# Kernel optimization log

Measured on AMD Instinct MI355X. Metric: run time of the kernel, lower is better.

## Reference

```python
import jax, jax.numpy as jnp
import numpy as np

B, D, T = 8, 256, 8192
N_Q, BINS = 8, 1024
COMMIT_W = 0.25

def setup_inputs() -> dict:
    key = jax.random.key(0)
    k1, k2 = jax.random.split(key)
    x = jax.random.normal(k1, (B, D, T), dtype=jnp.float32)
    codebooks = jax.random.normal(k2, (N_Q, BINS, D), dtype=jnp.float32)
    return {"x": x, "sample_rate": 16000, "codebooks": codebooks}

def _rvq(x_btd, codebooks):
    # x_btd: [B, T, D]; codebooks: [n_q, bins, D]
    def step(residual, cb):
        # nearest codebook entry under squared euclidean distance
        dots = jnp.einsum('btd,kd->btk', residual, cb)          # [B, T, K]
        cb_sq = jnp.sum(cb * cb, axis=-1)                        # [K]
        dist = cb_sq[None, None, :] - 2.0 * dots                 # argmin-equivalent distance
        idx = jnp.argmin(dist, axis=-1)                          # [B, T] int32
        q = cb[idx]                                              # [B, T, D] gather
        # commitment loss (codebook side detached, EnCodec style)
        loss = COMMIT_W * jnp.mean((jax.lax.stop_gradient(q) - residual) ** 2)
        # straight-through estimator
        q_ste = residual + jax.lax.stop_gradient(q - residual)
        return residual - q_ste, (q_ste, idx, loss)

    _, (qs, codes, losses) = jax.lax.scan(step, x_btd, codebooks)
    quantized = jnp.sum(qs, axis=0)                              # [B, T, D]
    return quantized, codes, losses

def reference(x, sample_rate, codebooks):
    n_q = codebooks.shape[0]
    bins = codebooks.shape[1]
    x_btd = jnp.transpose(x, (0, 2, 1))                          # [B, T, D]
    quantized_btd, codes, losses = _rvq(x_btd, codebooks)
    quantized = jnp.transpose(quantized_btd, (0, 2, 1))          # [B, D, T]
    bw_per_q = np.log2(bins) * sample_rate / 1000.0
    bw = jnp.asarray(n_q * bw_per_q, dtype=x.dtype)
    commit_loss = jnp.mean(losses)
    return quantized, codes, bw, commit_loss
```

## Files before the change

### kernel.cpp

```cpp
#include <hip/hip_runtime.h>
#include <math.h>

typedef _Float16 f16;
typedef f16 f16x8 __attribute__((ext_vector_type(8)));
typedef float f32x4 __attribute__((ext_vector_type(4)));

#define B_ 8
#define D_ 256
#define T_ 8192
#define NQ 8
#define KB 1024
#define TT 64
#define NTHR 512

#define OUT_CODES (B_ * D_ * T_)
#define OUT_BW (OUT_CODES + NQ * B_ * T_)
#define OUT_LOSS (OUT_BW + 1)

#define R_BYTES 65536
#define RED_OFF R_BYTES
#define REDI_OFF (RED_OFF + 1024)
#define WSUM_OFF (REDI_OFF + 1024)
#define LDS_TOTAL (WSUM_OFF + 32)

#define WS_HI (8192 * 4)
#define CBW_HALVES (NQ * 8 * KB * 32)
#define WS_LO (WS_HI + CBW_HALVES * 2)

__global__ void init_cbsq_kernel(const float* __restrict__ cb, const int* __restrict__ sr,
                                 float* __restrict__ csq, float* __restrict__ out) {
    int gid = blockIdx.x * blockDim.x + threadIdx.x;
    int row = gid >> 6;
    int lane = gid & 63;
    float4 v = ((const float4*)(cb + (size_t)row * D_))[lane];
    float s = fmaf(v.x, v.x, fmaf(v.y, v.y, fmaf(v.z, v.z, v.w * v.w)));
#pragma unroll
    for (int off = 32; off; off >>= 1) s += __shfl_down(s, off);
    if (lane == 0) csq[row] = s;
    if (gid == 0) {
        out[OUT_BW] = (float)(*sr) * (80.0f / 1000.0f);
        out[OUT_LOSS] = 0.0f;
    }
}

__global__ void init_split_kernel(const float* __restrict__ cb, f16* __restrict__ whi,
                                  f16* __restrict__ wlo) {
    int gid = blockIdx.x * 256 + threadIdx.x;
    int qdc = gid >> 10, k = gid & 1023;
    int q = qdc >> 3, dc = qdc & 7;
    const float* src = cb + ((size_t)(q * 1024 + k)) * 256 + dc * 32;
    size_t wo = (size_t)gid * 32;
#pragma unroll
    for (int jj = 0; jj < 4; ++jj) {
        float4 a = ((const float4*)src)[jj * 2];
        float4 c = ((const float4*)src)[jj * 2 + 1];
        float vals[8] = {a.x, a.y, a.z, a.w, c.x, c.y, c.z, c.w};
        f16x8 hv, lv;
#pragma unroll
        for (int i = 0; i < 8; ++i) {
            f16 h = (f16)vals[i];
            hv[i] = h;
            lv[i] = (f16)(vals[i] - (float)h);
        }
        *(f16x8*)&whi[wo + jj * 8] = hv;
        *(f16x8*)&wlo[wo + jj * 8] = lv;
    }
}

extern "C" __global__ __launch_bounds__(NTHR, 4)
void rvq_kernel(const float* __restrict__ x, const float* __restrict__ cb,
                const float* __restrict__ csq, const f16* __restrict__ whi,
                const f16* __restrict__ wlo, float* __restrict__ out) {
    extern __shared__ char smem[];
    f16* rs = (f16*)smem;
    float* redv = (float*)(smem + RED_OFF);
    int* redi = (int*)(smem + REDI_OFF);
    float* wsum = (float*)(smem + WSUM_OFF);

    const int tid = threadIdx.x;
    const int w = tid >> 6;
    const int l = tid & 63;
    const int l15 = l & 15;
    const int q4 = l >> 4;
    const int wm = w >> 2;
    const int wn = w & 3;

    const int b = blockIdx.x >> 7;
    const int t0 = (blockIdx.x & 127) * TT;
    const float* xb = x + (size_t)b * D_ * T_;

    for (int d = tid >> 6; d < D_; d += 8) {
        float v = xb[(size_t)d * T_ + t0 + l];
        f16 h = (f16)v;
        const int sw = l & 7;
        rs[l * 512 + (((d >> 3) ^ sw) << 3) + (d & 7)] = h;
        rs[l * 512 + ((((d >> 3) + 32) ^ sw) << 3) + (d & 7)] = (f16)(v - (float)h);
    }

    float ssq = 0.0f;

    for (int q = 0; q < NQ; ++q) {
        const float* cbq = cb + (size_t)q * KB * D_;
        const char* wq = (const char*)(whi + (size_t)q * 8 * KB * 32);
        const char* lq = (const char*)(wlo + (size_t)q * 8 * KB * 32);

        __syncthreads();

        float bval[8];
        int bidx[8];
#pragma unroll
        for (int e = 0; e < 8; ++e) { bval[e] = INFINITY; bidx[e] = 0; }

        const int swA = l15 & 7;

        for (int s = 0; s < 4; ++s) {
            const int vbase = ((s * 256 + wn * 64 + l15) << 6) + q4 * 16;

            f32x4 ah[2][4];
#pragma unroll
            for (int mt = 0; mt < 2; ++mt)
#pragma unroll
                for (int nt = 0; nt < 4; ++nt) ah[mt][nt] = (f32x4)0.0f;

#pragma unroll 1
            for (int dc = 0; dc < 8; ++dc) {
                const int ga = dc * 4 + q4;
                f16x8 af1[2], af2[2];
#pragma unroll
                for (int mt = 0; mt < 2; ++mt) {
                    const f16* rowp = rs + (wm * 32 + mt * 16 + l15) * 512;
                    af1[mt] = *(const f16x8*)&rowp[(ga ^ swA) << 3];
                    af2[mt] = *(const f16x8*)&rowp[((ga + 32) ^ swA) << 3];
                }
                const char* wqd = wq + dc * 65536;
                const char* lqd = lq + dc * 65536;
#pragma unroll
                for (int nt = 0; nt < 4; ++nt) {
                    const int off = vbase + nt * 1024;
                    const f16x8 cb1 = *(const f16x8*)(wqd + off);
                    const f16x8 cb2 = *(const f16x8*)(lqd + off);
#pragma unroll
                    for (int mt = 0; mt < 2; ++mt) {
                        ah[mt][nt] = __builtin_amdgcn_mfma_f32_16x16x32_f16(af1[mt], cb1, ah[mt][nt], 0, 0, 0);
                        ah[mt][nt] = __builtin_amdgcn_mfma_f32_16x16x32_f16(af2[mt], cb1, ah[mt][nt], 0, 0, 0);
                        ah[mt][nt] = __builtin_amdgcn_mfma_f32_16x16x32_f16(af1[mt], cb2, ah[mt][nt], 0, 0, 0);
                    }
                }
            }
            const int cbase = s * 256 + wn * 64 + l15;
#pragma unroll
            for (int nt = 0; nt < 4; ++nt) {
                const int code = cbase + nt * 16;
                const float cq = csq[q * KB + code];
#pragma unroll
                for (int mt = 0; mt < 2; ++mt)
#pragma unroll
                    for (int rg = 0; rg < 4; ++rg) {
                        const float dist = fmaf(-2.0f, ah[mt][nt][rg], cq);
                        const int e = mt * 4 + rg;
                        if (dist < bval[e]) { bval[e] = dist; bidx[e] = code; }
                    }
            }
        }
#pragma unroll
        for (int m = 1; m < 16; m <<= 1) {
#pragma unroll
            for (int e = 0; e < 8; ++e) {
                const float ov = __shfl_xor(bval[e], m);
                const int oi = __shfl_xor(bidx[e], m);
                if (ov < bval[e] || (ov == bval[e] && oi < bidx[e])) { bval[e] = ov; bidx[e] = oi; }
            }
        }
        if (l15 == 0) {
#pragma unroll
            for (int mt = 0; mt < 2; ++mt)
#pragma unroll
                for (int rg = 0; rg < 4; ++rg) {
                    const int tl = mt * 16 + q4 * 4 + rg;
                    redv[w * 32 + tl] = bval[mt * 4 + rg];
                    redi[w * 32 + tl] = bidx[mt * 4 + rg];
                }
        }
        __syncthreads();
        {
            const int t = tid & 63, ch = tid >> 6;
            const int wmr = t >> 5, tl = t & 31;
            float bv = redv[(wmr * 4) * 32 + tl];
            int bi = redi[(wmr * 4) * 32 + tl];
#pragma unroll
            for (int w2 = 1; w2 < 4; ++w2) {
                const float v = redv[(wmr * 4 + w2) * 32 + tl];
                const int ii = redi[(wmr * 4 + w2) * 32 + tl];
                if (v < bv || (v == bv && ii < bi)) { bv = v; bi = ii; }
            }
            if (ch == 0) out[OUT_CODES + ((size_t)q * B_ + b) * T_ + t0 + t] = (float)bi;
            const float* crow = cbq + (size_t)bi * D_ + ch * 32;
            f16* rowp = rs + t * 512;
            const int sw = t & 7;
#pragma unroll
            for (int jj = 0; jj < 4; ++jj) {
                const int g = ch * 4 + jj;
                const int g1 = (g ^ sw) << 3;
                const int g2 = ((g + 32) ^ sw) << 3;
                f16x8 hv = *(const f16x8*)&rowp[g1];
                f16x8 lv = *(const f16x8*)&rowp[g2];
                const float4 c0 = ((const float4*)crow)[jj * 2];
                const float4 c1 = ((const float4*)crow)[jj * 2 + 1];
                const float cc[8] = {c0.x, c0.y, c0.z, c0.w, c1.x, c1.y, c1.z, c1.w};
                f16x8 nh, nl;
#pragma unroll
                for (int i = 0; i < 8; ++i) {
                    const float r = (float)hv[i] + (float)lv[i];
                    const float nv = r - cc[i];
                    ssq = fmaf(nv, nv, ssq);
                    const f16 h = (f16)nv;
                    nh[i] = h;
                    nl[i] = (f16)(nv - (float)h);
                }
                *(f16x8*)&rowp[g1] = nh;
                *(f16x8*)&rowp[g2] = nl;
            }
        }
    }
    __syncthreads();
    {
        float* outq = out + (size_t)b * D_ * T_;
        for (int d = tid >> 6; d < D_; d += 8) {
            const int sw = l & 7;
            const float h1 = (float)rs[l * 512 + (((d >> 3) ^ sw) << 3) + (d & 7)];
            const float h2 = (float)rs[l * 512 + ((((d >> 3) + 32) ^ sw) << 3) + (d & 7)];
            const size_t gi = (size_t)d * T_ + t0 + l;
            outq[gi] = xb[gi] - (h1 + h2);
        }
    }
#pragma unroll
    for (int off = 32; off; off >>= 1) ssq += __shfl_down(ssq, off);
    if (l == 0) wsum[w] = ssq;
    __syncthreads();
    if (tid == 0) {
        float tot = 0.0f;
#pragma unroll
        for (int i = 0; i < 8; ++i) tot += wsum[i];
        const float scale = 0.25f / ((float)NQ * (float)B_ * (float)D_ * (float)T_);
        atomicAdd(out + OUT_LOSS, tot * scale);
    }
}

extern "C" void kernel_launch(void* const* d_in, const int* in_sizes, int n_in,
                              void* d_out, int out_size, void* d_ws, size_t ws_size,
                              hipStream_t stream) {
    const float* x = (const float*)d_in[0];
    const int* sr = (const int*)d_in[1];
    const float* cb = (const float*)d_in[2];
    float* out = (float*)d_out;
    float* csq = (float*)d_ws;
    f16* whi = (f16*)((char*)d_ws + WS_HI);
    f16* wlo = (f16*)((char*)d_ws + WS_LO);

    hipFuncSetAttribute((const void*)rvq_kernel, hipFuncAttributeMaxDynamicSharedMemorySize,
                        LDS_TOTAL);

    init_cbsq_kernel<<<2048, 256, 0, stream>>>(cb, sr, csq, out);
    init_split_kernel<<<256, 256, 0, stream>>>(cb, whi, wlo);
    rvq_kernel<<<B_ * (T_ / TT), NTHR, LDS_TOTAL, stream>>>(x, cb, csq, whi, wlo, out);
}
```

Measured before the change: 1.183 ms.

## Software-pipeline codebook fragment loads and shrink per-wave code tile

The code loop is restructured so each step covers 32 codes per wave (8 steps) instead of 64 (4 steps), halving the accumulator count. Codebook fragments for the next d-chunk are loaded from global memory while the current chunk's MFMAs run, hiding load latency. The codebook squared-norm loads are hoisted to the start of each step. This raises per-thread register use for the prefetch buffers and adds loop overhead from the doubled step count.

```diff
diff --git a/kernel.cpp b/kernel.cpp
--- a/kernel.cpp
+++ b/kernel.cpp
@@ -113,17 +113,36 @@
 
         const int swA = l15 & 7;
 
-        for (int s = 0; s < 4; ++s) {
-            const int vbase = ((s * 256 + wn * 64 + l15) << 6) + q4 * 16;
-
-            f32x4 ah[2][4];
+#pragma unroll 1
+        for (int s = 0; s < 8; ++s) {
+            const int code0 = s * 128 + wn * 32 + l15;
+            const int vb0 = (code0 << 6) + q4 * 16;
+            const int vb1 = vb0 + 1024;
+            const float cq0 = csq[q * KB + code0];
+            const float cq1 = csq[q * KB + code0 + 16];
+
+            f32x4 ah[2][2];
 #pragma unroll
             for (int mt = 0; mt < 2; ++mt)
 #pragma unroll
-                for (int nt = 0; nt < 4; ++nt) ah[mt][nt] = (f32x4)0.0f;
+                for (int nt = 0; nt < 2; ++nt) ah[mt][nt] = (f32x4)0.0f;
+
+            f16x8 c0h = *(const f16x8*)(wq + vb0);
+            f16x8 c0l = *(const f16x8*)(lq + vb0);
+            f16x8 c1h = *(const f16x8*)(wq + vb1);
+            f16x8 c1l = *(const f16x8*)(lq + vb1);
 
 #pragma unroll 1
             for (int dc = 0; dc < 8; ++dc) {
+                f16x8 n0h, n0l, n1h, n1l;
+                if (dc < 7) {
+                    const char* wd = wq + (dc + 1) * 65536;
+                    const char* ld = lq + (dc + 1) * 65536;
+                    n0h = *(const f16x8*)(wd + vb0);
+                    n0l = *(const f16x8*)(ld + vb0);
+                    n1h = *(const f16x8*)(wd + vb1);
+                    n1l = *(const f16x8*)(ld + vb1);
+                }
                 const int ga = dc * 4 + q4;
                 f16x8 af1[2], af2[2];
 #pragma unroll
@@ -132,26 +151,21 @@
                     af1[mt] = *(const f16x8*)&rowp[(ga ^ swA) << 3];
                     af2[mt] = *(const f16x8*)&rowp[((ga + 32) ^ swA) << 3];
                 }
-                const char* wqd = wq + dc * 65536;
-                const char* lqd = lq + dc * 65536;
-#pragma unroll
-                for (int nt = 0; nt < 4; ++nt) {
-                    const int off = vbase + nt * 1024;
-                    const f16x8 cb1 = *(const f16x8*)(wqd + off);
-                    const f16x8 cb2 = *(const f16x8*)(lqd + off);
-#pragma unroll
-                    for (int mt = 0; mt < 2; ++mt) {
-                        ah[mt][nt] = __builtin_amdgcn_mfma_f32_16x16x32_f16(af1[mt], cb1, ah[mt][nt], 0, 0, 0);
-                        ah[mt][nt] = __builtin_amdgcn_mfma_f32_16x16x32_f16(af2[mt], cb1, ah[mt][nt], 0, 0, 0);
-                        ah[mt][nt] = __builtin_amdgcn_mfma_f32_16x16x32_f16(af1[mt], cb2, ah[mt][nt], 0, 0, 0);
-                    }
-                }
-            }
-            const int cbase = s * 256 + wn * 64 + l15;
-#pragma unroll
-            for (int nt = 0; nt < 4; ++nt) {
-                const int code = cbase + nt * 16;
-                const float cq = csq[q * KB + code];
+#pragma unroll
+                for (int mt = 0; mt < 2; ++mt) {
+                    ah[mt][0] = __builtin_amdgcn_mfma_f32_16x16x32_f16(af1[mt], c0h, ah[mt][0], 0, 0, 0);
+                    ah[mt][0] = __builtin_amdgcn_mfma_f32_16x16x32_f16(af2[mt], c0h, ah[mt][0], 0, 0, 0);
+                    ah[mt][0] = __builtin_amdgcn_mfma_f32_16x16x32_f16(af1[mt], c0l, ah[mt][0], 0, 0, 0);
+                    ah[mt][1] = __builtin_amdgcn_mfma_f32_16x16x32_f16(af1[mt], c1h, ah[mt][1], 0, 0, 0);
+                    ah[mt][1] = __builtin_amdgcn_mfma_f32_16x16x32_f16(af2[mt], c1h, ah[mt][1], 0, 0, 0);
+                    ah[mt][1] = __builtin_amdgcn_mfma_f32_16x16x32_f16(af1[mt], c1l, ah[mt][1], 0, 0, 0);
+                }
+                if (dc < 7) { c0h = n0h; c0l = n0l; c1h = n1h; c1l = n1l; }
+            }
+#pragma unroll
+            for (int nt = 0; nt < 2; ++nt) {
+                const int code = code0 + nt * 16;
+                const float cq = nt ? cq1 : cq0;
 #pragma unroll
                 for (int mt = 0; mt < 2; ++mt)
 #pragma unroll
```

Measured after the change: 1.150 ms. -2.7%, faster.
